# Kernel optimization log

Measured on AMD Instinct MI355X. Metric: run time of the kernel, lower is better.

Reference implementation:

```python
import jax, jax.numpy as jnp
import numpy as np


def setup_inputs() -> dict:
    key = jax.random.key(0)
    ks = jax.random.split(key, 7)
    B, D, T, H = 32, 512, 4096, 512
    return {
        "query": jax.random.normal(ks[0], (B, D, 1), dtype=jnp.float32),
        "keys": jax.random.normal(ks[1], (B, D, T), dtype=jnp.float32),
        "values": jax.random.normal(ks[2], (B, D, T), dtype=jnp.float32),
        "w42": 0.01 * jax.random.normal(ks[3], (H, 2 * D), dtype=jnp.float32),
        "b4": 0.01 * jax.random.normal(ks[4], (H, 1), dtype=jnp.float32),
        "w54": 0.01 * jax.random.normal(ks[5], (1, H), dtype=jnp.float32),
        "b5": 0.01 * jax.random.normal(ks[6], (1, 1), dtype=jnp.float32),
    }


def reference(query, keys, values, w42, b4, w54, b5):
    D = keys.shape[1]
    # cat([keys, query.repeat T], dim=1) then w42 @ cat ==
    # w42[:, :D] @ keys + w42[:, D:] @ query (broadcast over T)
    n4 = (jnp.einsum('hd,bdt->bht', w42[:, :D], keys)
          + jnp.einsum('hd,bdo->bho', w42[:, D:], query)  # [B,H,1], broadcasts over T
          + b4)                                            # [H,1] broadcasts
    a4 = jnp.tanh(n4)                                      # [B,H,T]
    n5 = jnp.einsum('oh,bht->bot', w54, a4) + b5           # [B,1,T]
    # transpose(1,2) -> [B,T,1], softmax over dim=1 (T)
    a5 = jax.nn.softmax(n5[:, 0, :], axis=-1)              # [B,T]
    a6 = jnp.einsum('bvt,bt->bv', values, a5)[..., None]   # [B,Dv,1]
    return a6
```

## Files before the change

kernel.cpp:

```cpp
#include <hip/hip_runtime.h>
#include <hip/hip_bf16.h>
#include <cstdint>
#include <cstddef>

typedef __attribute__((ext_vector_type(4))) float f32x4;
typedef __attribute__((ext_vector_type(8))) short s16x8;
typedef __attribute__((ext_vector_type(8))) unsigned short u16x8;

#define NB 32
#define DD 512
#define TT 4096
#define HH 512
#define NKK 16

__device__ __forceinline__ unsigned short f2bf(float f) {
  uint32_t u = __builtin_bit_cast(uint32_t, f);
  u += 0x7fffu + ((u >> 16) & 1u);
  return (unsigned short)(u >> 16);
}

__device__ __forceinline__ uint32_t cvtpk(float a, float b) {
  uint32_t d;
  asm("v_cvt_pk_bf16_f32 %0, %1, %2" : "=v"(d) : "v"(a), "v"(b));
  return d;
}

__device__ __forceinline__ float tanh_fast(float x) {
  x = fminf(fmaxf(x, -15.f), 15.f);
  float e = __expf(2.f * x);
  return (e - 1.f) / (e + 1.f);
}

__global__ void kConvT(const float* __restrict__ w42, u16x8* __restrict__ W1swz) {
  int g = blockIdx.x * 256 + threadIdx.x;
  int h = g & 511, sk = g >> 9;
  int kk = sk >> 2, s = sk & 3;
  const float* src = &w42[h * 1024 + kk * 32 + s * 8];
  f32x4 v0 = *reinterpret_cast<const f32x4*>(src);
  f32x4 v1 = *reinterpret_cast<const f32x4*>(src + 4);
  u16x8 c;
  c[0] = f2bf(v0.x); c[1] = f2bf(v0.y); c[2] = f2bf(v0.z); c[3] = f2bf(v0.w);
  c[4] = f2bf(v1.x); c[5] = f2bf(v1.y); c[6] = f2bf(v1.z); c[7] = f2bf(v1.w);
  W1swz[kk * 2048 + s * 512 + h] = c;
}

__global__ void kQterm(const float* __restrict__ w42, const float* __restrict__ query,
                       const float* __restrict__ b4, float* __restrict__ qterm) {
  int wid = blockIdx.x * 4 + (threadIdx.x >> 6);
  int lane = threadIdx.x & 63;
  int b = wid >> 9, h = wid & 511;
  const float* wr = &w42[h * 1024 + 512];
  const float* q  = &query[b * 512];
  int d = lane * 8;
  f32x4 w0 = *(const f32x4*)&wr[d], w1 = *(const f32x4*)&wr[d + 4];
  f32x4 q0 = *(const f32x4*)&q[d],  q1 = *(const f32x4*)&q[d + 4];
  float s = w0.x*q0.x + w0.y*q0.y + w0.z*q0.z + w0.w*q0.w
          + w1.x*q1.x + w1.y*q1.y + w1.z*q1.z + w1.w*q1.w;
  #pragma unroll
  for (int off = 32; off; off >>= 1) s += __shfl_xor(s, off);
  if (lane == 0) qterm[b * 512 + h] = s + b4[h];
}

__global__ __launch_bounds__(256, 3) void kGemmE(
    const float* __restrict__ keys, const u16x8* __restrict__ W1swz,
    const float* __restrict__ qterm, const float* __restrict__ w54,
    float* __restrict__ n5p) {
  __shared__ s16x8 Bs[2][512];
  __shared__ float red[2][128];

  int p = blockIdx.x;
  int lix = (p & 7) * 512 + (p >> 3);
  int hq = lix & 3, tt = (lix >> 2) & 31, b = lix >> 7;
  int h0 = hq * 128, t0 = tt * 128;

  int tid = threadIdx.x, lane = tid & 63, wid = tid >> 6;
  int wh = wid & 1, wt = wid >> 1;
  int lr = lane & 15, lg = lane >> 4;

  int s = tid >> 6, ta = tid & 63;
  const float* kp = keys + (size_t)b * DD * TT + (size_t)(s * 8) * TT + t0 + ta;
  int wiA = s * 128 + (ta ^ s), wiB = s * 128 + ((ta + 64) ^ s);
  const s16x8* ap = reinterpret_cast<const s16x8*>(W1swz) + lg * 512 + h0 + wh * 64 + lr;
  int rci[4];
  #pragma unroll
  for (int n = 0; n < 4; ++n) {
    int t = wt * 64 + n * 16 + lr;
    rci[n] = lg * 128 + (t ^ lg);
  }

  f32x4 acc[4][4];
  #pragma unroll
  for (int m = 0; m < 4; ++m)
    #pragma unroll
    for (int n = 0; n < 4; ++n) acc[m][n] = (f32x4){0.f, 0.f, 0.f, 0.f};

  float r[16];
  #pragma unroll
  for (int j = 0; j < 8; ++j) r[j] = kp[(size_t)j * TT];
  #pragma unroll
  for (int j = 0; j < 8; ++j) r[8 + j] = kp[(size_t)j * TT + 64];

  #pragma unroll
  for (int kk = 0; kk < NKK; ++kk) {
    const int cur = kk & 1;
    s16x8 af[4];
    #pragma unroll
    for (int m = 0; m < 4; ++m) af[m] = ap[kk * 2048 + m * 16];

    union { uint32_t u[4]; s16x8 v; } ca, cb;
    #pragma unroll
    for (int j = 0; j < 4; ++j) {
      ca.u[j] = cvtpk(r[2 * j], r[2 * j + 1]);
      cb.u[j] = cvtpk(r[8 + 2 * j], r[9 + 2 * j]);
    }
    Bs[cur][wiA] = ca.v;
    Bs[cur][wiB] = cb.v;

    if (kk + 1 < NKK) {
      const float* kp2 = kp + (size_t)(kk + 1) * 32 * TT;
      #pragma unroll
      for (int j = 0; j < 8; ++j) r[j] = kp2[(size_t)j * TT];
      #pragma unroll
      for (int j = 0; j < 8; ++j) r[8 + j] = kp2[(size_t)j * TT + 64];
    }

    asm volatile("s_waitcnt lgkmcnt(0)" ::: "memory");
    __builtin_amdgcn_s_barrier();

    s16x8 bf[4];
    #pragma unroll
    for (int n = 0; n < 4; ++n) bf[n] = Bs[cur][rci[n]];

    #pragma unroll
    for (int m = 0; m < 4; ++m)
      #pragma unroll
      for (int n = 0; n < 4; ++n)
        acc[m][n] = __builtin_amdgcn_mfma_f32_16x16x32_bf16(af[m], bf[n], acc[m][n], 0, 0, 0);
  }

  float part[4] = {0.f, 0.f, 0.f, 0.f};
  #pragma unroll
  for (int m = 0; m < 4; ++m) {
    #pragma unroll
    for (int rr = 0; rr < 4; ++rr) {
      int h = h0 + wh * 64 + m * 16 + lg * 4 + rr;
      float qv = qterm[b * HH + h];
      float wvv = w54[h];
      #pragma unroll
      for (int n = 0; n < 4; ++n)
        part[n] += wvv * tanh_fast(acc[m][n][rr] + qv);
    }
  }
  #pragma unroll
  for (int n = 0; n < 4; ++n) {
    part[n] += __shfl_xor(part[n], 16);
    part[n] += __shfl_xor(part[n], 32);
  }
  if (lane < 16) {
    #pragma unroll
    for (int n = 0; n < 4; ++n) red[wh][wt * 64 + n * 16 + lane] = part[n];
  }
  __syncthreads();
  if (tid < 128) {
    float v = red[0][tid] + red[1][tid];
    n5p[((size_t)hq * NB + b) * TT + t0 + tid] = v;
  }
}

__global__ void kSoftE(const float* __restrict__ n5p, float* __restrict__ e,
                       float* __restrict__ Zinv) {
  int b = blockIdx.x, tid = threadIdx.x;
  int lane = tid & 63, wid = tid >> 6;
  __shared__ float zsh[4];
  float z = 0.f;
  #pragma unroll
  for (int i = 0; i < 16; ++i) {
    int t = tid + i * 256;
    float v = n5p[(0 * NB + b) * TT + t] + n5p[(1 * NB + b) * TT + t]
            + n5p[(2 * NB + b) * TT + t] + n5p[(3 * NB + b) * TT + t];
    float ev = __expf(v);
    e[b * TT + t] = ev;
    z += ev;
  }
  #pragma unroll
  for (int off = 32; off; off >>= 1) z += __shfl_xor(z, off);
  if (lane == 0) zsh[wid] = z;
  __syncthreads();
  if (tid == 0) Zinv[b] = 1.f / (zsh[0] + zsh[1] + zsh[2] + zsh[3]);
}

__global__ void kOut(const float* __restrict__ values, const float* __restrict__ e,
                     const float* __restrict__ Zinv, float* __restrict__ out) {
  int blk = blockIdx.x;
  int b = blk >> 7;
  int wid = threadIdx.x >> 6, lane = threadIdx.x & 63;
  int v = (blk & 127) * 4 + wid;
  const float* row = &values[((size_t)b * 512 + v) * TT];
  const float* wv = &e[b * TT];
  float s0 = 0.f, s1 = 0.f, s2 = 0.f, s3 = 0.f;
  #pragma unroll
  for (int i = 0; i < 16; ++i) {
    int t = (i * 64 + lane) * 4;
    f32x4 x = __builtin_nontemporal_load(reinterpret_cast<const f32x4*>(&row[t]));
    f32x4 y = *(const f32x4*)&wv[t];
    float d = x.x * y.x + x.y * y.y + x.z * y.z + x.w * y.w;
    if ((i & 3) == 0) s0 += d; else if ((i & 3) == 1) s1 += d;
    else if ((i & 3) == 2) s2 += d; else s3 += d;
  }
  float s = (s0 + s1) + (s2 + s3);
  #pragma unroll
  for (int off = 32; off; off >>= 1) s += __shfl_xor(s, off);
  if (lane == 0) out[b * 512 + v] = s * Zinv[b];
}

extern "C" void kernel_launch(void* const* d_in, const int* in_sizes, int n_in,
                              void* d_out, int out_size, void* d_ws, size_t ws_size,
                              hipStream_t stream) {
  const float* query  = (const float*)d_in[0];
  const float* keys   = (const float*)d_in[1];
  const float* values = (const float*)d_in[2];
  const float* w42    = (const float*)d_in[3];
  const float* b4     = (const float*)d_in[4];
  const float* w54    = (const float*)d_in[5];
  float* out = (float*)d_out;

  char* ws = (char*)d_ws;
  u16x8* W1swz = (u16x8*)ws;
  float* qterm = (float*)(ws + (512 << 10));
  float* Zinv  = (float*)(ws + (576 << 10));
  float* e     = (float*)(ws + (640 << 10));
  float* n5p   = (float*)(ws + (1152 << 10));

  kConvT <<<128, 256, 0, stream>>>(w42, W1swz);
  kQterm <<<4096, 256, 0, stream>>>(w42, query, b4, qterm);
  kGemmE <<<4096, 256, 0, stream>>>(keys, W1swz, qterm, w54, n5p);
  kSoftE <<<32, 256, 0, stream>>>(n5p, e, Zinv);
  kOut   <<<4096, 256, 0, stream>>>(values, e, Zinv, out);
}
```

Before: 184.0 us.

## Retile keys GEMM to 128x256 tiles with shared-memory staged weights

The main GEMM kernel now gives each block a 128(h) x 256(t) tile instead of 128x128, and launches half as many blocks. Each wave owns 64 t-columns and all 128 h-rows, so the cross-wave reduction through shared memory and its extra barrier go away. The bf16 weight tile is staged through shared memory with double buffering instead of being read by every wave from global memory. Keys are fetched as float4 nontemporal loads with a new swizzle. The cost is higher register pressure from 32 accumulators per lane, with launch bounds dropped from 3 to 2 blocks per CU, which lowers occupancy.

Result: slower. 209.2 us (+13.7%).

```diff
diff --git a/kernel.cpp b/kernel.cpp
--- a/kernel.cpp
+++ b/kernel.cpp
@@ -61,78 +61,84 @@
   if (lane == 0) qterm[b * 512 + h] = s + b4[h];
 }
 
-__global__ __launch_bounds__(256, 3) void kGemmE(
+__global__ __launch_bounds__(256, 2) void kGemmE(
     const float* __restrict__ keys, const u16x8* __restrict__ W1swz,
     const float* __restrict__ qterm, const float* __restrict__ w54,
     float* __restrict__ n5p) {
-  __shared__ s16x8 Bs[2][512];
-  __shared__ float red[2][128];
+  __shared__ s16x8 Asb[2 * 512];
+  __shared__ s16x8 Bsb[2 * 1024];
 
   int p = blockIdx.x;
-  int lix = (p & 7) * 512 + (p >> 3);
-  int hq = lix & 3, tt = (lix >> 2) & 31, b = lix >> 7;
-  int h0 = hq * 128, t0 = tt * 128;
-
-  int tid = threadIdx.x, lane = tid & 63, wid = tid >> 6;
-  int wh = wid & 1, wt = wid >> 1;
+  int xcd = p & 7, local = p >> 3;
+  int hq = local & 3, g = local >> 2;
+  int pair = xcd * 64 + g;
+  int b = pair >> 4, tc = pair & 15;
+  int tG = tc * 256;
+
+  int tid = threadIdx.x, lane = tid & 63, w = tid >> 6;
   int lr = lane & 15, lg = lane >> 4;
 
-  int s = tid >> 6, ta = tid & 63;
-  const float* kp = keys + (size_t)b * DD * TT + (size_t)(s * 8) * TT + t0 + ta;
-  int wiA = s * 128 + (ta ^ s), wiB = s * 128 + ((ta + 64) ^ s);
-  const s16x8* ap = reinterpret_cast<const s16x8*>(W1swz) + lg * 512 + h0 + wh * 64 + lr;
-  int rci[4];
-  #pragma unroll
-  for (int n = 0; n < 4; ++n) {
-    int t = wt * 64 + n * 16 + lr;
-    rci[n] = lg * 128 + (t ^ lg);
-  }
-
-  f32x4 acc[4][4];
-  #pragma unroll
-  for (int m = 0; m < 4; ++m)
+  int u = lane;
+  const float* kpB = keys + (size_t)b * DD * TT + (size_t)(w * 8) * TT + tG + u * 4;
+  const u16x8* apG0 = W1swz + (size_t)(tid >> 7) * 512 + hq * 128 + (tid & 127);
+  const u16x8* apG1 = W1swz + (size_t)((tid + 256) >> 7) * 512 + hq * 128 + (tid & 127);
+
+  int cW[4];
+  #pragma unroll
+  for (int dt = 0; dt < 4; ++dt) cW[dt] = w * 256 + dt * 64 + (u ^ (dt << 1) ^ w);
+  int rciB[4];
+  #pragma unroll
+  for (int n = 0; n < 4; ++n)
+    rciB[n] = lg * 256 + (lr & 3) * 64 +
+              ((w * 16 + n * 4 + (lr >> 2)) ^ ((lr & 3) << 1) ^ lg);
+
+  f32x4 acc[8][4];
+  #pragma unroll
+  for (int m = 0; m < 8; ++m)
     #pragma unroll
     for (int n = 0; n < 4; ++n) acc[m][n] = (f32x4){0.f, 0.f, 0.f, 0.f};
 
-  float r[16];
-  #pragma unroll
-  for (int j = 0; j < 8; ++j) r[j] = kp[(size_t)j * TT];
-  #pragma unroll
-  for (int j = 0; j < 8; ++j) r[8 + j] = kp[(size_t)j * TT + 64];
+  u16x8 ra0, ra1;
+  f32x4 rb[8];
+  ra0 = apG0[0]; ra1 = apG1[0];
+  #pragma unroll
+  for (int j = 0; j < 8; ++j)
+    rb[j] = __builtin_nontemporal_load(reinterpret_cast<const f32x4*>(&kpB[(size_t)j * TT]));
 
   #pragma unroll
   for (int kk = 0; kk < NKK; ++kk) {
     const int cur = kk & 1;
-    s16x8 af[4];
-    #pragma unroll
-    for (int m = 0; m < 4; ++m) af[m] = ap[kk * 2048 + m * 16];
-
-    union { uint32_t u[4]; s16x8 v; } ca, cb;
-    #pragma unroll
-    for (int j = 0; j < 4; ++j) {
-      ca.u[j] = cvtpk(r[2 * j], r[2 * j + 1]);
-      cb.u[j] = cvtpk(r[8 + 2 * j], r[9 + 2 * j]);
+    *reinterpret_cast<u16x8*>(&Asb[(cur << 9) + tid])       = ra0;
+    *reinterpret_cast<u16x8*>(&Asb[(cur << 9) + tid + 256]) = ra1;
+    #pragma unroll
+    for (int dt = 0; dt < 4; ++dt) {
+      union { uint32_t q[4]; s16x8 v; } c;
+      #pragma unroll
+      for (int jj = 0; jj < 4; ++jj)
+        c.q[jj] = cvtpk(rb[2 * jj][dt], rb[2 * jj + 1][dt]);
+      Bsb[(cur << 10) + cW[dt]] = c.v;
     }
-    Bs[cur][wiA] = ca.v;
-    Bs[cur][wiB] = cb.v;
-
     if (kk + 1 < NKK) {
-      const float* kp2 = kp + (size_t)(kk + 1) * 32 * TT;
-      #pragma unroll
-      for (int j = 0; j < 8; ++j) r[j] = kp2[(size_t)j * TT];
-      #pragma unroll
-      for (int j = 0; j < 8; ++j) r[8 + j] = kp2[(size_t)j * TT + 64];
+      ra0 = apG0[(kk + 1) * 2048];
+      ra1 = apG1[(kk + 1) * 2048];
+      const float* kp2 = kpB + (size_t)(kk + 1) * 32 * TT;
+      #pragma unroll
+      for (int j = 0; j < 8; ++j)
+        rb[j] = __builtin_nontemporal_load(reinterpret_cast<const f32x4*>(&kp2[(size_t)j * TT]));
     }
-
     asm volatile("s_waitcnt lgkmcnt(0)" ::: "memory");
     __builtin_amdgcn_s_barrier();
 
-    s16x8 bf[4];
-    #pragma unroll
-    for (int n = 0; n < 4; ++n) bf[n] = Bs[cur][rci[n]];
-
-    #pragma unroll
-    for (int m = 0; m < 4; ++m)
+    s16x8 af[8], bf[4];
+    const s16x8* Ab = &Asb[cur << 9];
+    #pragma unroll
+    for (int m = 0; m < 8; ++m) af[m] = Ab[lg * 128 + m * 16 + lr];
+    const s16x8* Bb = &Bsb[cur << 10];
+    #pragma unroll
+    for (int n = 0; n < 4; ++n) bf[n] = Bb[rciB[n]];
+
+    #pragma unroll
+    for (int m = 0; m < 8; ++m)
       #pragma unroll
       for (int n = 0; n < 4; ++n)
         acc[m][n] = __builtin_amdgcn_mfma_f32_16x16x32_bf16(af[m], bf[n], acc[m][n], 0, 0, 0);
@@ -140,15 +146,15 @@
 
   float part[4] = {0.f, 0.f, 0.f, 0.f};
   #pragma unroll
-  for (int m = 0; m < 4; ++m) {
+  for (int m = 0; m < 8; ++m) {
     #pragma unroll
     for (int rr = 0; rr < 4; ++rr) {
-      int h = h0 + wh * 64 + m * 16 + lg * 4 + rr;
+      int h = hq * 128 + m * 16 + lg * 4 + rr;
       float qv = qterm[b * HH + h];
-      float wvv = w54[h];
+      float wv = w54[h];
       #pragma unroll
       for (int n = 0; n < 4; ++n)
-        part[n] += wvv * tanh_fast(acc[m][n][rr] + qv);
+        part[n] += wv * tanh_fast(acc[m][n][rr] + qv);
     }
   }
   #pragma unroll
@@ -158,12 +164,8 @@
   }
   if (lane < 16) {
     #pragma unroll
-    for (int n = 0; n < 4; ++n) red[wh][wt * 64 + n * 16 + lane] = part[n];
-  }
-  __syncthreads();
-  if (tid < 128) {
-    float v = red[0][tid] + red[1][tid];
-    n5p[((size_t)hq * NB + b) * TT + t0 + tid] = v;
+    for (int n = 0; n < 4; ++n)
+      n5p[((size_t)hq * NB + b) * TT + tG + w * 64 + n * 16 + lane] = part[n];
   }
 }
 
@@ -233,7 +235,7 @@
 
   kConvT <<<128, 256, 0, stream>>>(w42, W1swz);
   kQterm <<<4096, 256, 0, stream>>>(w42, query, b4, qterm);
-  kGemmE <<<4096, 256, 0, stream>>>(keys, W1swz, qterm, w54, n5p);
+  kGemmE <<<2048, 256, 0, stream>>>(keys, W1swz, qterm, w54, n5p);
   kSoftE <<<32, 256, 0, stream>>>(n5p, e, Zinv);
   kOut   <<<4096, 256, 0, stream>>>(values, e, Zinv, out);
 }
```
